# Kernel optimization log

Measured on AMD Instinct MI355X. Metric: run time of the kernel, lower is better.

## Reference

```python
import jax, jax.numpy as jnp
import numpy as np
from jax import lax

B, C, H, W, NH = 16, 512, 32, 32, 8
HC = C // NH  # head channels = 64


def setup_inputs() -> dict:
    key = jax.random.key(0)
    ks = jax.random.split(key, 8)
    rn = lambda i, shape, scale: jax.random.normal(ks[i], shape, jnp.float32) * scale
    return dict(
        image=jax.random.normal(ks[0], (B, C, H, W), jnp.float32),
        watermark=jax.random.normal(ks[1], (B, C, H, W), jnp.float32),
        img_ln_w=jnp.ones((C, H, W), jnp.float32),
        img_ln_b=jnp.zeros((C, H, W), jnp.float32),
        wm_ln_w=jnp.ones((C, H, W), jnp.float32),
        wm_ln_b=jnp.zeros((C, H, W), jnp.float32),
        img_pw_w=rn(2, (3 * C, C), 0.02),
        img_pw_b=jnp.zeros((3 * C,), jnp.float32),
        img_dw_w=rn(3, (3 * C, 3, 3, 3), 0.1),
        img_dw_b=jnp.zeros((3 * C,), jnp.float32),
        wm_pw_w=rn(4, (3 * C, C), 0.02),
        wm_pw_b=jnp.zeros((3 * C,), jnp.float32),
        wm_dw_w=rn(5, (3 * C, 3, 3, 3), 0.1),
        wm_dw_b=jnp.zeros((3 * C,), jnp.float32),
        proj=rn(6, (2 * C, C), 0.02),
    )


def _layernorm(x, w, b, eps=1e-5):
    # LayerNorm over [C,H,W] per sample, elementwise affine of shape [C,H,W]
    mu = jnp.mean(x, axis=(1, 2, 3), keepdims=True)
    var = jnp.mean((x - mu) ** 2, axis=(1, 2, 3), keepdims=True)
    return (x - mu) * lax.rsqrt(var + eps) * w + b


def _dconv_proj(x, pw_w, pw_b, dw_w, dw_b):
    # pointwise 1x1 conv C -> 3C
    x = jnp.einsum('bchw,oc->bohw', x, pw_w) + pw_b[None, :, None, None]
    # depthwise 3x3 conv on 3C channels with groups=C (3 channels per group)
    x = lax.conv_general_dilated(
        x, dw_w, window_strides=(1, 1), padding='SAME',
        dimension_numbers=('NCHW', 'OIHW', 'NCHW'), feature_group_count=C)
    x = x + dw_b[None, :, None, None]
    return jnp.split(x, 3, axis=1)  # Q, K, V each [B,C,H,W]


def reference(image, watermark, img_ln_w, img_ln_b, wm_ln_w, wm_ln_b,
              img_pw_w, img_pw_b, img_dw_w, img_dw_b,
              wm_pw_w, wm_pw_b, wm_dw_w, wm_dw_b, proj):
    img = _layernorm(image, img_ln_w, img_ln_b)
    wm = _layernorm(watermark, wm_ln_w, wm_ln_b)
    Qi, Ki, Vi = _dconv_proj(img, img_pw_w, img_pw_b, img_dw_w, img_dw_b)
    Qw, Kw, Vw = _dconv_proj(wm, wm_pw_w, wm_pw_b, wm_dw_w, wm_dw_b)
    r = lambda t: t.reshape(B, NH, HC, H * W)
    Qi, Ki, Vi, Qw, Kw, Vw = map(r, (Qi, Ki, Vi, Qw, Kw, Vw))
    # NOTE: original code calls F.normalize but discards the result -> no-op.
    Kc = jnp.concatenate([Ki, Kw], axis=2)  # [B,NH,2*HC,HW]
    Vc = jnp.concatenate([Vi, Vw], axis=2)  # [B,NH,2*HC,HW]
    # scores: K_concat @ Q^T over the HW axis -> [B,NH,2*HC,HC], softmax over HC
    Ai = jax.nn.softmax(jnp.einsum('bnkp,bnqp->bnkq', Kc, Qi), axis=-1)
    Aw = jax.nn.softmax(jnp.einsum('bnkp,bnqp->bnkq', Kc, Qw), axis=-1)
    # A^T @ V_concat -> [B,NH,HC,HW]
    img_attn = jnp.einsum('bnkq,bnkp->bnqp', Ai, Vc)
    wm_attn = jnp.einsum('bnkq,bnkp->bnqp', Aw, Vc)
    attn = jnp.concatenate([img_attn, wm_attn], axis=2).reshape(B, 2 * C, H, W)
    # final channel-mixing projection: [B,H,W,2C] @ [2C,C] -> [B,C,H,W]
    return jnp.einsum('bdhw,dc->bchw', attn, proj)
```

## Files before the change

kernel.cpp:

```cpp
#include <hip/hip_runtime.h>
#include <hip/hip_bf16.h>
#include <stdint.h>

#define Bn  16
#define Cch 512
#define C3  1536
#define HWp 1024

typedef __attribute__((ext_vector_type(8))) short bf16x8;
typedef __attribute__((ext_vector_type(4))) float f32x4;

#define DEV static __device__ __forceinline__

DEV float bflo(unsigned u) { return __builtin_bit_cast(float, u << 16); }
DEV float bfhi(unsigned u) { return __builtin_bit_cast(float, u & 0xffff0000u); }
DEV unsigned short f2bf(float f) {
  __hip_bfloat16 h = __float2bfloat16(f);
  return __builtin_bit_cast(unsigned short, h);
}

DEV void async16(__hip_bfloat16* lds, const __hip_bfloat16* g) {
  __builtin_amdgcn_global_load_lds(
      (const __attribute__((address_space(1))) unsigned*)g,
      (__attribute__((address_space(3))) unsigned*)lds, 16, 0, 0);
}

__global__ __launch_bounds__(256) void k_prep(
    const float* __restrict__ img_pw_w, const float* __restrict__ wm_pw_w,
    const float* __restrict__ proj,
    __hip_bfloat16* __restrict__ Wpw, __hip_bfloat16* __restrict__ projT)
{
  int i = blockIdx.x * 256 + threadIdx.x;
  const int NW = C3 * Cch;
  if (i < NW)          Wpw[i] = __float2bfloat16(img_pw_w[i]);
  else if (i < 2 * NW) Wpw[i] = __float2bfloat16(wm_pw_w[i - NW]);
  else {
    int j = i - 2 * NW;
    int c = j >> 10, d = j & 1023;
    projT[(size_t)c * 1024 + d] = __float2bfloat16(proj[(size_t)d * 512 + c]);
  }
}

__global__ __launch_bounds__(256) void k_ln_partial(
    const float* __restrict__ image, const float* __restrict__ watermark,
    float* __restrict__ part)
{
  int blk = blockIdx.x;
  int chunk = blk & 63, b = (blk >> 6) & 15, t = blk >> 10;
  const float* x = (t ? watermark : image) + (size_t)b * Cch * HWp + chunk * 8192;
  const float4* xv = (const float4*)x;
  float s = 0.f, ss = 0.f;
#pragma unroll
  for (int i = 0; i < 8; i++) {
    float4 v = xv[threadIdx.x + i * 256];
    s  += v.x + v.y + v.z + v.w;
    ss += v.x * v.x + v.y * v.y + v.z * v.z + v.w * v.w;
  }
#pragma unroll
  for (int off = 32; off; off >>= 1) { s += __shfl_down(s, off); ss += __shfl_down(ss, off); }
  __shared__ float ls[4], lss[4];
  int wv = threadIdx.x >> 6;
  if ((threadIdx.x & 63) == 0) { ls[wv] = s; lss[wv] = ss; }
  __syncthreads();
  if (threadIdx.x == 0) {
    part[blk * 2]     = ls[0] + ls[1] + ls[2] + ls[3];
    part[blk * 2 + 1] = lss[0] + lss[1] + lss[2] + lss[3];
  }
}

__global__ void k_ln_final(const float* __restrict__ part, float* __restrict__ stats)
{
  int i = threadIdx.x;
  if (i < 32) {
    float S = 0.f, SS = 0.f;
    for (int c2 = 0; c2 < 64; c2++) { S += part[(i * 64 + c2) * 2]; SS += part[(i * 64 + c2) * 2 + 1]; }
    const float inv = 1.f / (float)(Cch * HWp);
    float mu  = S * inv;
    float var = SS * inv - mu * mu;
    stats[i]      = mu;
    stats[32 + i] = rsqrtf(var + 1e-5f);
  }
}

__global__ __launch_bounds__(256) void k_norm_t(
    const float* __restrict__ image, const float* __restrict__ watermark,
    const float* __restrict__ img_w, const float* __restrict__ img_b,
    const float* __restrict__ wm_w,  const float* __restrict__ wm_b,
    const float* __restrict__ stats, __hip_bfloat16* __restrict__ xnT)
{
  int blk = blockIdx.x;
  int ct = blk & 15, pt = (blk >> 4) & 31, b = (blk >> 9) & 15, t = blk >> 13;
  const float* x   = (t ? watermark : image) + (size_t)b * Cch * HWp;
  const float* wgt = t ? wm_w : img_w;
  const float* bia = t ? wm_b : img_b;
  float mu = stats[t * 16 + b], rstd = stats[32 + t * 16 + b];
  __shared__ float tile[32][33];
  int pl = threadIdx.x & 31, cl0 = threadIdx.x >> 5;
  int p = pt * 32 + pl;
#pragma unroll
  for (int k = 0; k < 4; k++) {
    int cl = cl0 + k * 8;
    int idx = (ct * 32 + cl) * HWp + p;
    tile[cl][pl] = (x[idx] - mu) * rstd * wgt[idx] + bia[idx];
  }
  __syncthreads();
  __hip_bfloat16* dst = xnT + ((size_t)(t * 16 + b)) * HWp * Cch;
#pragma unroll
  for (int k = 0; k < 4; k++) {
    int prow = cl0 + k * 8;
    dst[(size_t)(pt * 32 + prow) * Cch + ct * 32 + pl] = __float2bfloat16(tile[pl][prow]);
  }
}

template<int Kdim, int Ncols, bool OBF, bool HB>
DEV void gemm_core(const __hip_bfloat16* __restrict__ A,
                   const __hip_bfloat16* __restrict__ Bt,
                   const float* __restrict__ bias, void* __restrict__ Cout)
{
  __shared__ __hip_bfloat16 As[128 * 64];
  __shared__ __hip_bfloat16 Bs[128 * 64];
  const int tid = threadIdx.x, lane = tid & 63, wv = tid >> 6;
  const int lr = lane & 15, lq = lane >> 4;
  const int wm = (wv >> 1) * 64, wn = (wv & 1) * 64;
  const int m0 = blockIdx.y * 128, n0 = blockIdx.x * 128;
  f32x4 acc[4][4] = {};
  const int srow = tid >> 3, sseg = (tid & 7) * 8;
  for (int k0 = 0; k0 < Kdim; k0 += 64) {
#pragma unroll
    for (int c = 0; c < 4; c++) {
      int row = srow + c * 32;
      async16(&As[row * 64 + sseg], &A [(size_t)(m0 + row) * Kdim + k0 + sseg]);
      async16(&Bs[row * 64 + sseg], &Bt[(size_t)(n0 + row) * Kdim + k0 + sseg]);
    }
    __syncthreads();
#pragma unroll
    for (int ks = 0; ks < 2; ks++) {
      bf16x8 af[4], bfr[4];
#pragma unroll
      for (int mi = 0; mi < 4; mi++)
        af[mi]  = *(const bf16x8*)&As[(wm + mi * 16 + lr) * 64 + ks * 32 + lq * 8];
#pragma unroll
      for (int ni = 0; ni < 4; ni++)
        bfr[ni] = *(const bf16x8*)&Bs[(wn + ni * 16 + lr) * 64 + ks * 32 + lq * 8];
#pragma unroll
      for (int mi = 0; mi < 4; mi++)
#pragma unroll
        for (int ni = 0; ni < 4; ni++)
          acc[mi][ni] = __builtin_amdgcn_mfma_f32_16x16x32_bf16(af[mi], bfr[ni], acc[mi][ni], 0, 0, 0);
    }
    __syncthreads();
  }
#pragma unroll
  for (int mi = 0; mi < 4; mi++) {
    int mrow = m0 + wm + mi * 16 + lq * 4;
#pragma unroll
    for (int ni = 0; ni < 4; ni++) {
      int ncol = n0 + wn + ni * 16 + lr;
#pragma unroll
      for (int r = 0; r < 4; r++) {
        float y = acc[mi][ni][r];
        int row = mrow + r;
        if (HB) y += bias[row];
        if (OBF) ((__hip_bfloat16*)Cout)[(size_t)row * Ncols + ncol] = __float2bfloat16(y);
        else     ((float*)Cout)[(size_t)row * Ncols + ncol] = y;
      }
    }
  }
}

__global__ __launch_bounds__(256) void k_pw_gemm(
    const __hip_bfloat16* __restrict__ Wpw, const __hip_bfloat16* __restrict__ xnT,
    const float* __restrict__ img_pw_b, const float* __restrict__ wm_pw_b,
    __hip_bfloat16* __restrict__ Y)
{
  int bz = blockIdx.z, t = bz >> 4;
  gemm_core<512, 1024, true, true>(
      Wpw + (size_t)t * C3 * Cch,
      xnT + (size_t)bz * HWp * Cch,
      t ? wm_pw_b : img_pw_b,
      Y + (size_t)bz * C3 * HWp);
}

__global__ __launch_bounds__(256) void k_proj_gemm(
    const __hip_bfloat16* __restrict__ projT, const __hip_bfloat16* __restrict__ attnT,
    float* __restrict__ out)
{
  int b = blockIdx.z;
  gemm_core<1024, 1024, false, false>(
      projT, attnT + (size_t)b * HWp * 1024, nullptr, out + (size_t)b * Cch * HWp);
}

__global__ __launch_bounds__(256) void k_dw(
    const __hip_bfloat16* __restrict__ Y,
    const float* __restrict__ img_dw_w, const float* __restrict__ img_dw_b,
    const float* __restrict__ wm_dw_w,  const float* __restrict__ wm_dw_b,
    __hip_bfloat16* __restrict__ QKV)
{
  int idx = blockIdx.x * 256 + threadIdx.x;
  int w0 = (idx & 3) * 8;
  int h  = (idx >> 2) & 31;
  int g  = __builtin_amdgcn_readfirstlane((idx >> 7) & 511);
  int tb = __builtin_amdgcn_readfirstlane(idx >> 16);
  int t  = tb >> 4;
  const float* dww = (t ? wm_dw_w : img_dw_w) + g * 81;
  const float* dwb = (t ? wm_dw_b : img_dw_b) + g * 3;
  const __hip_bfloat16* base = Y + ((size_t)tb * C3 + g * 3) * HWp;
  float acc[3][8];
#pragma unroll
  for (int o = 0; o < 3; o++) {
    float bv = dwb[o];
#pragma unroll
    for (int w = 0; w < 8; w++) acc[o][w] = bv;
  }
  const bool mlo = (w0 == 0), mhi = (w0 == 24);
#pragma unroll
  for (int i = 0; i < 3; i++) {
#pragma unroll
    for (int kh = 0; kh < 3; kh++) {
      int hh = h + kh - 1;
      if ((unsigned)hh > 31u) continue;
      const unsigned* up = (const unsigned*)(base + i * HWp + hh * 32 + (w0 - 2));
      float v[12];
#pragma unroll
      for (int d2 = 0; d2 < 6; d2++) { unsigned u = up[d2]; v[d2*2] = bflo(u); v[d2*2+1] = bfhi(u); }
      if (mlo) { v[0] = 0.f; v[1] = 0.f; }
      if (mhi) { v[10] = 0.f; v[11] = 0.f; }
#pragma unroll
      for (int o = 0; o < 3; o++) {
        float wk0 = dww[o*27 + i*9 + kh*3 + 0];
        float wk1 = dww[o*27 + i*9 + kh*3 + 1];
        float wk2 = dww[o*27 + i*9 + kh*3 + 2];
#pragma unroll
        for (int w = 0; w < 8; w++)
          acc[o][w] += v[w + 1] * wk0 + v[w + 2] * wk1 + v[w + 3] * wk2;
      }
    }
  }
#pragma unroll
  for (int o = 0; o < 3; o++) {
    union { unsigned short us[8]; uint4 v4; } pk;
#pragma unroll
    for (int w = 0; w < 8; w++) pk.us[w] = f2bf(acc[o][w]);
    *(uint4*)(QKV + ((size_t)tb * C3 + g * 3 + o) * HWp + h * 32 + w0) = pk.v4;
  }
}

__global__ __launch_bounds__(256) void k_attn_scores(
    const __hip_bfloat16* __restrict__ QKV, __hip_bfloat16* __restrict__ ATg)
{
  int bn = blockIdx.x, b = bn >> 3, nh = bn & 7;
  int tid = threadIdx.x, lane = tid & 63, wv = tid >> 6;
  int lr = lane & 15, lq = lane >> 4;
  const __hip_bfloat16* kbase[2];
#pragma unroll
  for (int kt = 0; kt < 2; kt++) {
    int krow = wv * 32 + kt * 16 + lr;
    int tk = krow >> 6, hc = krow & 63;
    kbase[kt] = QKV + (((size_t)(tk * 16 + b)) * C3 + 512 + nh * 64 + hc) * HWp + lq * 8;
  }
  const __hip_bfloat16* qbase[2][4];
#pragma unroll
  for (int m = 0; m < 2; m++)
#pragma unroll
    for (int qt = 0; qt < 4; qt++)
      qbase[m][qt] = QKV + (((size_t)(m * 16 + b)) * C3 + nh * 64 + qt * 16 + lr) * HWp + lq * 8;

  f32x4 acc[2][2][4] = {};
  for (int p0 = 0; p0 < HWp; p0 += 32) {
    bf16x8 af[2];
#pragma unroll
    for (int kt = 0; kt < 2; kt++) af[kt] = *(const bf16x8*)(kbase[kt] + p0);
#pragma unroll
    for (int m = 0; m < 2; m++)
#pragma unroll
      for (int qt = 0; qt < 4; qt++) {
        bf16x8 bq = *(const bf16x8*)(qbase[m][qt] + p0);
#pragma unroll
        for (int kt = 0; kt < 2; kt++)
          acc[m][kt][qt] = __builtin_amdgcn_mfma_f32_16x16x32_bf16(af[kt], bq, acc[m][kt][qt], 0, 0, 0);
      }
  }
  __shared__ float SbufT[2][64][128];
#pragma unroll
  for (int m = 0; m < 2; m++)
#pragma unroll
    for (int kt = 0; kt < 2; kt++)
#pragma unroll
      for (int qt = 0; qt < 4; qt++)
#pragma unroll
        for (int r = 0; r < 4; r++)
          SbufT[m][qt * 16 + lr][wv * 32 + kt * 16 + lq * 4 + r] = acc[m][kt][qt][r];
  __syncthreads();
  int m = tid >> 7, k = tid & 127;
  float vals[64], mx = -1e30f;
#pragma unroll
  for (int q = 0; q < 64; q++) { vals[q] = SbufT[m][q][k]; mx = fmaxf(mx, vals[q]); }
  float ssum = 0.f;
#pragma unroll
  for (int q = 0; q < 64; q++) { vals[q] = __expf(vals[q] - mx); ssum += vals[q]; }
  float inv = 1.f / ssum;
  __hip_bfloat16* outp = ATg + ((size_t)(bn * 2 + m)) * 64 * 128 + k;
#pragma unroll
  for (int q = 0; q < 64; q++) outp[(size_t)q * 128] = __float2bfloat16(vals[q] * inv);
}

__global__ __launch_bounds__(256) void k_attn_out(
    const __hip_bfloat16* __restrict__ QKV, const __hip_bfloat16* __restrict__ ATg,
    __hip_bfloat16* __restrict__ attnT)
{
  int blk = blockIdx.x, pc = blk & 3, bn = blk >> 2, b = bn >> 3, nh = bn & 7;
  int tid = threadIdx.x, lane = tid & 63, wv = tid >> 6;
  int lr = lane & 15, lq = lane >> 4;
  __shared__ __hip_bfloat16 ATs[64][136];
  __shared__ __hip_bfloat16 VTs[64][136];
  for (int m = 0; m < 2; m++) {
    __syncthreads();
    {
      const __hip_bfloat16* src = ATg + ((size_t)(bn * 2 + m)) * 64 * 128;
#pragma unroll
      for (int s = 0; s < 4; s++) {
        int id = tid + s * 256, row = id >> 4, seg = (id & 15) * 8;
        *(uint4*)&ATs[row][seg] = *(const uint4*)&src[row * 128 + seg];
      }
    }
    for (int ps = 0; ps < 4; ps++) {
      int p0 = pc * 256 + ps * 64;
      __syncthreads();
#pragma unroll
      for (int s = 0; s < 4; s++) {
        int id = tid + s * 256;
        int k = id >> 3, seg = (id & 7) * 8;
        int tk = k >> 6, hc = k & 63;
        const __hip_bfloat16* vp =
            QKV + (((size_t)(tk * 16 + b)) * C3 + 1024 + nh * 64 + hc) * HWp + p0 + seg;
        uint4 pkv = *(const uint4*)vp;
        unsigned short* pv = (unsigned short*)&pkv;
#pragma unroll
        for (int e = 0; e < 8; e++) *(unsigned short*)&VTs[seg + e][k] = pv[e];
      }
      __syncthreads();
      f32x4 oacc[4] = {};
#pragma unroll
      for (int ks = 0; ks < 4; ks++) {
        bf16x8 bv = *(const bf16x8*)&VTs[wv * 16 + lr][ks * 32 + lq * 8];
#pragma unroll
        for (int qt = 0; qt < 4; qt++) {
          bf16x8 av = *(const bf16x8*)&ATs[qt * 16 + lr][ks * 32 + lq * 8];
          oacc[qt] = __builtin_amdgcn_mfma_f32_16x16x32_bf16(av, bv, oacc[qt], 0, 0, 0);
        }
      }
#pragma unroll
      for (int qt = 0; qt < 4; qt++) {
        int q = qt * 16 + lq * 4;
        int d = nh * 128 + m * 64 + q;
        int p = p0 + wv * 16 + lr;
        union { unsigned short us[4]; uint2 v2; } pk;
#pragma unroll
        for (int r = 0; r < 4; r++) pk.us[r] = f2bf(oacc[qt][r]);
        *(uint2*)&attnT[((size_t)b * HWp + p) * 1024 + d] = pk.v2;
      }
    }
  }
}

extern "C" void kernel_launch(void* const* d_in, const int* in_sizes, int n_in,
                              void* d_out, int out_size, void* d_ws, size_t ws_size,
                              hipStream_t stream)
{
  (void)in_sizes; (void)n_in; (void)out_size; (void)ws_size;
  const float* image     = (const float*)d_in[0];
  const float* watermark = (const float*)d_in[1];
  const float* img_ln_w  = (const float*)d_in[2];
  const float* img_ln_b  = (const float*)d_in[3];
  const float* wm_ln_w   = (const float*)d_in[4];
  const float* wm_ln_b   = (const float*)d_in[5];
  const float* img_pw_w  = (const float*)d_in[6];
  const float* img_pw_b  = (const float*)d_in[7];
  const float* img_dw_w  = (const float*)d_in[8];
  const float* img_dw_b  = (const float*)d_in[9];
  const float* wm_pw_w   = (const float*)d_in[10];
  const float* wm_pw_b   = (const float*)d_in[11];
  const float* wm_dw_w   = (const float*)d_in[12];
  const float* wm_dw_b   = (const float*)d_in[13];
  const float* proj      = (const float*)d_in[14];

  char* ws = (char*)d_ws;
  __hip_bfloat16* Wpw    = (__hip_bfloat16*)(ws + 0);
  __hip_bfloat16* projT  = (__hip_bfloat16*)(ws + 3145728);
  float*          lnpart = (float*)(ws + 4194304);
  float*          stats  = (float*)(ws + 4210688);
  __hip_bfloat16* xnT    = (__hip_bfloat16*)(ws + 5242880);
  __hip_bfloat16* attnT  = xnT;
  __hip_bfloat16* Y      = (__hip_bfloat16*)(ws + 41943040);
  __hip_bfloat16* ATg    = Y;
  __hip_bfloat16* QKV    = (__hip_bfloat16*)(ws + 142606336);

  k_prep<<<8192, 256, 0, stream>>>(img_pw_w, wm_pw_w, proj, Wpw, projT);
  k_ln_partial<<<2048, 256, 0, stream>>>(image, watermark, lnpart);
  k_ln_final<<<1, 64, 0, stream>>>(lnpart, stats);
  k_norm_t<<<16384, 256, 0, stream>>>(image, watermark, img_ln_w, img_ln_b,
                                      wm_ln_w, wm_ln_b, stats, xnT);
  dim3 gpw(8, 12, 32);
  k_pw_gemm<<<gpw, 256, 0, stream>>>(Wpw, xnT, img_pw_b, wm_pw_b, Y);
  k_dw<<<8192, 256, 0, stream>>>(Y, img_dw_w, img_dw_b, wm_dw_w, wm_dw_b, QKV);
  k_attn_scores<<<128, 256, 0, stream>>>(QKV, ATg);
  k_attn_out<<<512, 256, 0, stream>>>(QKV, ATg, attnT);
  dim3 gpj(8, 4, 16);
  k_proj_gemm<<<gpj, 256, 0, stream>>>(projT, attnT, (float*)d_out);
}
```

Before: 400.1 us.

## Vectorize norm-transpose, split attention scores per query stream, shrink proj GEMM M-tile

```diff
diff --git a/kernel.cpp b/kernel.cpp
--- a/kernel.cpp
+++ b/kernel.cpp
@@ -89,61 +89,82 @@
     const float* __restrict__ stats, __hip_bfloat16* __restrict__ xnT)
 {
   int blk = blockIdx.x;
-  int ct = blk & 15, pt = (blk >> 4) & 31, b = (blk >> 9) & 15, t = blk >> 13;
+  int ct = blk & 15, pt = (blk >> 4) & 15, b = (blk >> 8) & 15, t = blk >> 12;
+  int c0 = ct * 32, p0 = pt * 64;
   const float* x   = (t ? watermark : image) + (size_t)b * Cch * HWp;
   const float* wgt = t ? wm_w : img_w;
   const float* bia = t ? wm_b : img_b;
   float mu = stats[t * 16 + b], rstd = stats[32 + t * 16 + b];
-  __shared__ float tile[32][33];
-  int pl = threadIdx.x & 31, cl0 = threadIdx.x >> 5;
-  int p = pt * 32 + pl;
-#pragma unroll
-  for (int k = 0; k < 4; k++) {
-    int cl = cl0 + k * 8;
-    int idx = (ct * 32 + cl) * HWp + p;
-    tile[cl][pl] = (x[idx] - mu) * rstd * wgt[idx] + bia[idx];
+  __shared__ float tile[32 * 66];
+  int tid = threadIdx.x;
+  {
+    int c = tid >> 3, s = tid & 7;
+    const float* xr = x   + (size_t)(c0 + c) * HWp + p0;
+    const float* wr = wgt + (size_t)(c0 + c) * HWp + p0;
+    const float* br = bia + (size_t)(c0 + c) * HWp + p0;
+#pragma unroll
+    for (int j = 0; j < 2; j++) {
+      int f = s + j * 8;
+      float4 xv = *(const float4*)&xr[f * 4];
+      float4 wv = *(const float4*)&wr[f * 4];
+      float4 bv = *(const float4*)&br[f * 4];
+      float n0 = (xv.x - mu) * rstd * wv.x + bv.x;
+      float n1 = (xv.y - mu) * rstd * wv.y + bv.y;
+      float n2 = (xv.z - mu) * rstd * wv.z + bv.z;
+      float n3 = (xv.w - mu) * rstd * wv.w + bv.w;
+      *(float2*)&tile[c * 66 + f * 4]     = make_float2(n0, n1);
+      *(float2*)&tile[c * 66 + f * 4 + 2] = make_float2(n2, n3);
+    }
   }
   __syncthreads();
-  __hip_bfloat16* dst = xnT + ((size_t)(t * 16 + b)) * HWp * Cch;
-#pragma unroll
-  for (int k = 0; k < 4; k++) {
-    int prow = cl0 + k * 8;
-    dst[(size_t)(pt * 32 + prow) * Cch + ct * 32 + pl] = __float2bfloat16(tile[pl][prow]);
-  }
-}
-
-template<int Kdim, int Ncols, bool OBF, bool HB>
+  {
+    int p = tid >> 2, cq = tid & 3;
+    union { unsigned short us[8]; uint4 v4; } pk;
+#pragma unroll
+    for (int j = 0; j < 8; j++) pk.us[j] = f2bf(tile[(cq * 8 + j) * 66 + p]);
+    __hip_bfloat16* dst = xnT + ((size_t)(t * 16 + b)) * HWp * Cch
+                        + (size_t)(p0 + p) * Cch + c0 + cq * 8;
+    *(uint4*)dst = pk.v4;
+  }
+}
+
+template<int MI, int Kdim, int Ncols, bool OBF, bool HB>
 DEV void gemm_core(const __hip_bfloat16* __restrict__ A,
                    const __hip_bfloat16* __restrict__ Bt,
                    const float* __restrict__ bias, void* __restrict__ Cout)
 {
-  __shared__ __hip_bfloat16 As[128 * 64];
+  constexpr int MT = MI * 32;
+  __shared__ __hip_bfloat16 As[MT * 64];
   __shared__ __hip_bfloat16 Bs[128 * 64];
   const int tid = threadIdx.x, lane = tid & 63, wv = tid >> 6;
   const int lr = lane & 15, lq = lane >> 4;
-  const int wm = (wv >> 1) * 64, wn = (wv & 1) * 64;
-  const int m0 = blockIdx.y * 128, n0 = blockIdx.x * 128;
-  f32x4 acc[4][4] = {};
+  const int wm = (wv >> 1) * (MI * 16), wn = (wv & 1) * 64;
+  const int m0 = blockIdx.y * MT, n0 = blockIdx.x * 128;
+  f32x4 acc[MI][4] = {};
   const int srow = tid >> 3, sseg = (tid & 7) * 8;
   for (int k0 = 0; k0 < Kdim; k0 += 64) {
 #pragma unroll
+    for (int c = 0; c < MI; c++) {
+      int row = srow + c * 32;
+      async16(&As[row * 64 + sseg], &A[(size_t)(m0 + row) * Kdim + k0 + sseg]);
+    }
+#pragma unroll
     for (int c = 0; c < 4; c++) {
       int row = srow + c * 32;
-      async16(&As[row * 64 + sseg], &A [(size_t)(m0 + row) * Kdim + k0 + sseg]);
       async16(&Bs[row * 64 + sseg], &Bt[(size_t)(n0 + row) * Kdim + k0 + sseg]);
     }
     __syncthreads();
 #pragma unroll
     for (int ks = 0; ks < 2; ks++) {
-      bf16x8 af[4], bfr[4];
-#pragma unroll
-      for (int mi = 0; mi < 4; mi++)
+      bf16x8 af[MI], bfr[4];
+#pragma unroll
+      for (int mi = 0; mi < MI; mi++)
         af[mi]  = *(const bf16x8*)&As[(wm + mi * 16 + lr) * 64 + ks * 32 + lq * 8];
 #pragma unroll
       for (int ni = 0; ni < 4; ni++)
         bfr[ni] = *(const bf16x8*)&Bs[(wn + ni * 16 + lr) * 64 + ks * 32 + lq * 8];
 #pragma unroll
-      for (int mi = 0; mi < 4; mi++)
+      for (int mi = 0; mi < MI; mi++)
 #pragma unroll
         for (int ni = 0; ni < 4; ni++)
           acc[mi][ni] = __builtin_amdgcn_mfma_f32_16x16x32_bf16(af[mi], bfr[ni], acc[mi][ni], 0, 0, 0);
@@ -151,7 +172,7 @@
     __syncthreads();
   }
 #pragma unroll
-  for (int mi = 0; mi < 4; mi++) {
+  for (int mi = 0; mi < MI; mi++) {
     int mrow = m0 + wm + mi * 16 + lq * 4;
 #pragma unroll
     for (int ni = 0; ni < 4; ni++) {
@@ -174,7 +195,7 @@
     __hip_bfloat16* __restrict__ Y)
 {
   int bz = blockIdx.z, t = bz >> 4;
-  gemm_core<512, 1024, true, true>(
+  gemm_core<4, 512, 1024, true, true>(
       Wpw + (size_t)t * C3 * Cch,
       xnT + (size_t)bz * HWp * Cch,
       t ? wm_pw_b : img_pw_b,
@@ -186,7 +207,7 @@
     float* __restrict__ out)
 {
   int b = blockIdx.z;
-  gemm_core<1024, 1024, false, false>(
+  gemm_core<2, 1024, 1024, false, false>(
       projT, attnT + (size_t)b * HWp * 1024, nullptr, out + (size_t)b * Cch * HWp);
 }
 
@@ -248,7 +269,8 @@
 __global__ __launch_bounds__(256) void k_attn_scores(
     const __hip_bfloat16* __restrict__ QKV, __hip_bfloat16* __restrict__ ATg)
 {
-  int bn = blockIdx.x, b = bn >> 3, nh = bn & 7;
+  int blk = blockIdx.x, m = blk & 1, bn = blk >> 1;
+  int b = bn >> 3, nh = bn & 7;
   int tid = threadIdx.x, lane = tid & 63, wv = tid >> 6;
   int lr = lane & 15, lq = lane >> 4;
   const __hip_bfloat16* kbase[2];
@@ -258,50 +280,50 @@
     int tk = krow >> 6, hc = krow & 63;
     kbase[kt] = QKV + (((size_t)(tk * 16 + b)) * C3 + 512 + nh * 64 + hc) * HWp + lq * 8;
   }
-  const __hip_bfloat16* qbase[2][4];
-#pragma unroll
-  for (int m = 0; m < 2; m++)
-#pragma unroll
-    for (int qt = 0; qt < 4; qt++)
-      qbase[m][qt] = QKV + (((size_t)(m * 16 + b)) * C3 + nh * 64 + qt * 16 + lr) * HWp + lq * 8;
-
-  f32x4 acc[2][2][4] = {};
+  const __hip_bfloat16* qbase[4];
+#pragma unroll
+  for (int qt = 0; qt < 4; qt++)
+    qbase[qt] = QKV + (((size_t)(m * 16 + b)) * C3 + nh * 64 + qt * 16 + lr) * HWp + lq * 8;
+
+  f32x4 acc[2][4] = {};
   for (int p0 = 0; p0 < HWp; p0 += 32) {
     bf16x8 af[2];
 #pragma unroll
     for (int kt = 0; kt < 2; kt++) af[kt] = *(const bf16x8*)(kbase[kt] + p0);
 #pragma unroll
-    for (int m = 0; m < 2; m++)
-#pragma unroll
-      for (int qt = 0; qt < 4; qt++) {
-        bf16x8 bq = *(const bf16x8*)(qbase[m][qt] + p0);
-#pragma unroll
-        for (int kt = 0; kt < 2; kt++)
-          acc[m][kt][qt] = __builtin_amdgcn_mfma_f32_16x16x32_bf16(af[kt], bq, acc[m][kt][qt], 0, 0, 0);
-      }
-  }
-  __shared__ float SbufT[2][64][128];
-#pragma unroll
-  for (int m = 0; m < 2; m++)
-#pragma unroll
-    for (int kt = 0; kt < 2; kt++)
-#pragma unroll
-      for (int qt = 0; qt < 4; qt++)
-#pragma unroll
-        for (int r = 0; r < 4; r++)
-          SbufT[m][qt * 16 + lr][wv * 32 + kt * 16 + lq * 4 + r] = acc[m][kt][qt][r];
+    for (int qt = 0; qt < 4; qt++) {
+      bf16x8 bq = *(const bf16x8*)(qbase[qt] + p0);
+#pragma unroll
+      for (int kt = 0; kt < 2; kt++)
+        acc[kt][qt] = __builtin_amdgcn_mfma_f32_16x16x32_bf16(af[kt], bq, acc[kt][qt], 0, 0, 0);
+    }
+  }
+  __shared__ float S[64][129];
+  __shared__ float red[2][2][128];
+#pragma unroll
+  for (int kt = 0; kt < 2; kt++)
+#pragma unroll
+    for (int qt = 0; qt < 4; qt++)
+#pragma unroll
+      for (int r = 0; r < 4; r++)
+        S[qt * 16 + lr][wv * 32 + kt * 16 + lq * 4 + r] = acc[kt][qt][r];
   __syncthreads();
-  int m = tid >> 7, k = tid & 127;
-  float vals[64], mx = -1e30f;
-#pragma unroll
-  for (int q = 0; q < 64; q++) { vals[q] = SbufT[m][q][k]; mx = fmaxf(mx, vals[q]); }
+  int k = tid & 127, qh = tid >> 7;
+  float vals[32], mx = -1e30f;
+#pragma unroll
+  for (int j = 0; j < 32; j++) { vals[j] = S[qh * 32 + j][k]; mx = fmaxf(mx, vals[j]); }
+  red[0][qh][k] = mx;
+  __syncthreads();
+  float M = fmaxf(red[0][0][k], red[0][1][k]);
   float ssum = 0.f;
 #pragma unroll
-  for (int q = 0; q < 64; q++) { vals[q] = __expf(vals[q] - mx); ssum += vals[q]; }
-  float inv = 1.f / ssum;
-  __hip_bfloat16* outp = ATg + ((size_t)(bn * 2 + m)) * 64 * 128 + k;
-#pragma unroll
-  for (int q = 0; q < 64; q++) outp[(size_t)q * 128] = __float2bfloat16(vals[q] * inv);
+  for (int j = 0; j < 32; j++) { vals[j] = __expf(vals[j] - M); ssum += vals[j]; }
+  red[1][qh][k] = ssum;
+  __syncthreads();
+  float inv = 1.f / (red[1][0][k] + red[1][1][k]);
+  __hip_bfloat16* outp = ATg + (((size_t)(bn * 2 + m)) * 64 + qh * 32) * 128 + k;
+#pragma unroll
+  for (int j = 0; j < 32; j++) outp[(size_t)j * 128] = __float2bfloat16(vals[j] * inv);
 }
 
 __global__ __launch_bounds__(256) void k_attn_out(
@@ -398,13 +420,13 @@
   k_prep<<<8192, 256, 0, stream>>>(img_pw_w, wm_pw_w, proj, Wpw, projT);
   k_ln_partial<<<2048, 256, 0, stream>>>(image, watermark, lnpart);
   k_ln_final<<<1, 64, 0, stream>>>(lnpart, stats);
-  k_norm_t<<<16384, 256, 0, stream>>>(image, watermark, img_ln_w, img_ln_b,
-                                      wm_ln_w, wm_ln_b, stats, xnT);
+  k_norm_t<<<8192, 256, 0, stream>>>(image, watermark, img_ln_w, img_ln_b,
+                                     wm_ln_w, wm_ln_b, stats, xnT);
   dim3 gpw(8, 12, 32);
   k_pw_gemm<<<gpw, 256, 0, stream>>>(Wpw, xnT, img_pw_b, wm_pw_b, Y);
   k_dw<<<8192, 256, 0, stream>>>(Y, img_dw_w, img_dw_b, wm_dw_w, wm_dw_b, QKV);
-  k_attn_scores<<<128, 256, 0, stream>>>(QKV, ATg);
+  k_attn_scores<<<256, 256, 0, stream>>>(QKV, ATg);
   k_attn_out<<<512, 256, 0, stream>>>(QKV, ATg, attnT);
-  dim3 gpj(8, 4, 16);
+  dim3 gpj(8, 8, 16);
   k_proj_gemm<<<gpj, 256, 0, stream>>>(projT, attnT, (float*)d_out);
 }
```

New measurement: 392.5 us. Within noise of the previous version (-1.9%).
